# Kernel optimization log

Measured on AMD Instinct MI355X. Metric: run time of the kernel, lower is better.

## Reference

```python
import jax, jax.numpy as jnp
import numpy as np

B, L, D_MODEL = 16, 2048, 512
S, D_LLM = 1000, 1024
H, E = 8, 64  # n_heads, d_keys
D_OUT = 64


def setup_inputs() -> dict:
    key = jax.random.key(0)
    ks = jax.random.split(key, 11)
    sc = lambda d: 1.0 / np.sqrt(d)
    return {
        "target_embedding": jax.random.normal(ks[0], (B, L, D_MODEL), dtype=jnp.float32),
        "source_embedding": jax.random.normal(ks[1], (S, D_LLM), dtype=jnp.float32),
        "value_embedding": jax.random.normal(ks[2], (S, D_LLM), dtype=jnp.float32),
        "Wq": jax.random.normal(ks[3], (D_MODEL, H * E), dtype=jnp.float32) * sc(D_MODEL),
        "bq": jnp.zeros((H * E,), dtype=jnp.float32),
        "Wk": jax.random.normal(ks[4], (D_LLM, H * E), dtype=jnp.float32) * sc(D_LLM),
        "bk": jnp.zeros((H * E,), dtype=jnp.float32),
        "Wv": jax.random.normal(ks[5], (D_LLM, H * E), dtype=jnp.float32) * sc(D_LLM),
        "bv": jnp.zeros((H * E,), dtype=jnp.float32),
        "Wo": jax.random.normal(ks[6], (H * E, D_OUT), dtype=jnp.float32) * sc(H * E),
        "bo": jnp.zeros((D_OUT,), dtype=jnp.float32),
    }


def reference(target_embedding, source_embedding, value_embedding,
              Wq, bq, Wk, bk, Wv, bv, Wo, bo):
    # projections
    q = (target_embedding @ Wq + bq).reshape(B, L, H, E)   # blhe
    k = (source_embedding @ Wk + bk).reshape(S, H, E)      # she
    v = (value_embedding @ Wv + bv).reshape(S, H, E)       # she
    scale = 1.0 / jnp.sqrt(jnp.asarray(E, dtype=q.dtype))
    scores = jnp.einsum("blhe,she->bhls", q, k)            # (B,H,L,S)
    A = jax.nn.softmax(scale * scores, axis=-1)            # dropout in eval mode = identity
    out = jnp.einsum("bhls,she->blhe", A, v).reshape(B, L, H * E)
    return out @ Wo + bo                                    # (B,L,64)
```

## Files before the change

### kernel.cpp

```cpp
#include <hip/hip_runtime.h>

typedef __attribute__((ext_vector_type(4))) float  f32x4;
typedef __attribute__((ext_vector_type(8))) __bf16 bf16x8;
typedef __attribute__((ext_vector_type(4))) __bf16 bf16x4;

static __device__ __forceinline__ f32x4 mfma16(bf16x8 a, bf16x8 b, f32x4 c) {
  return __builtin_amdgcn_mfma_f32_16x16x32_bf16(a, b, c, 0, 0, 0);
}

typedef __attribute__((address_space(1))) const unsigned int* gas1_t;
typedef __attribute__((address_space(3))) unsigned int* las3_t;
static __device__ __forceinline__ void glds16(const void* g, void* l) {
  __builtin_amdgcn_global_load_lds((gas1_t)g, (las3_t)l, 16, 0, 0);
}

#define QSCALE 0.18033688011112042f

__global__ __launch_bounds__(256) void prep_w(
    const float* __restrict__ Wq, const float* __restrict__ Wk,
    const float* __restrict__ Wv, const float* __restrict__ Wo,
    __bf16* __restrict__ wqT, __bf16* __restrict__ wkT,
    __bf16* __restrict__ wvT, __bf16* __restrict__ woT) {
  int i = blockIdx.x * 256 + threadIdx.x;
  if (i < 262144) {
    int k = i & 511, n = i >> 9;
    wqT[i] = (__bf16)Wq[k * 512 + n];
  } else if (i < 786432) {
    int j = i - 262144; int k = j & 1023, n = j >> 10;
    wkT[j] = (__bf16)Wk[k * 512 + n];
  } else if (i < 1310720) {
    int j = i - 786432; int k = j & 1023, n = j >> 10;
    wvT[j] = (__bf16)Wv[k * 512 + n];
  } else if (i < 1343488) {
    int j = i - 1310720; int k = j & 511, n = j >> 9;
    woT[j] = (__bf16)Wo[k * 64 + n];
  }
}

__global__ __launch_bounds__(256) void prep_cvt(
    const float* __restrict__ tgt, const float* __restrict__ src,
    const float* __restrict__ val,
    __bf16* __restrict__ tgtb, __bf16* __restrict__ srcb, __bf16* __restrict__ valb) {
  const int j = blockIdx.x * 256 + threadIdx.x;
  const int C0 = 32768 * 512 / 4;
  const int CV = 1024 * 1024 / 4;
  if (j < C0) {
    f32x4 v = *(const f32x4*)&tgt[(size_t)j * 4];
    bf16x4 o; o[0]=(__bf16)v[0]; o[1]=(__bf16)v[1]; o[2]=(__bf16)v[2]; o[3]=(__bf16)v[3];
    *(bf16x4*)&tgtb[(size_t)j * 4] = o;
  } else if (j < C0 + 2 * CV) {
    const int which = (j - C0) / CV;
    const int u = (j - C0) - which * CV;
    const float* in = which ? val : src;
    __bf16* outp = which ? valb : srcb;
    bf16x4 o;
    if (u * 4 < 1000 * 1024) {
      f32x4 v = *(const f32x4*)&in[(size_t)u * 4];
      o[0]=(__bf16)v[0]; o[1]=(__bf16)v[1]; o[2]=(__bf16)v[2]; o[3]=(__bf16)v[3];
    } else {
      o[0]=(__bf16)0.0f; o[1]=(__bf16)0.0f; o[2]=(__bf16)0.0f; o[3]=(__bf16)0.0f;
    }
    *(bf16x4*)&outp[(size_t)u * 4] = o;
  }
}

template <int MODE>
__global__ __launch_bounds__(256, 2) void gemm_bt(
    const __bf16* __restrict__ A, const __bf16* __restrict__ BT,
    const float* __restrict__ bias, float scale,
    __bf16* __restrict__ C, int M, int N, int K) {
  const int n0 = blockIdx.x * 128, m0 = blockIdx.y * 128;
  __shared__ __bf16 sA[128 * 32], sB[128 * 32];
  const int t = threadIdx.x;
  const int w = t >> 6, lane = t & 63;
  const int wr = w >> 1, wc = w & 1;
  const int lr = lane & 15, lg = lane >> 4;

  const int grow = w * 32 + (lane >> 2);
  const int lslot = (lane & 3) ^ ((lane >> 2) & 3) ^ (lane >> 4);
  char* const sAw = (char*)sA + w * 2048;
  char* const sBw = (char*)sB + w * 2048;

  const int rslot = (lg ^ (lr & 3) ^ ((lr >> 2) & 3)) << 4;
  const int aOff = wr * 4096 + lr * 64 + rslot;
  const int bOff = wc * 4096 + lr * 64 + rslot;

  f32x4 acc[4][4];
#pragma unroll
  for (int i = 0; i < 4; ++i)
#pragma unroll
    for (int j = 0; j < 4; ++j) acc[i][j] = f32x4{0.f, 0.f, 0.f, 0.f};

  const size_t gaBase0 = (size_t)(m0 + grow) * K + lslot * 8;
  const size_t gaBase1 = (size_t)(m0 + grow + 16) * K + lslot * 8;
  const size_t gbBase0 = (size_t)(n0 + grow) * K + lslot * 8;
  const size_t gbBase1 = (size_t)(n0 + grow + 16) * K + lslot * 8;

  for (int kc = 0; kc < K; kc += 32) {
    __syncthreads();
    glds16(&A[gaBase0 + kc], sAw);
    glds16(&A[gaBase1 + kc], sAw + 1024);
    glds16(&BT[gbBase0 + kc], sBw);
    glds16(&BT[gbBase1 + kc], sBw + 1024);
    __syncthreads();

    bf16x8 af[4], bfr[4];
#pragma unroll
    for (int i = 0; i < 4; ++i) {
      af[i]  = *(const bf16x8*)((const char*)sA + aOff + i * 1024);
      bfr[i] = *(const bf16x8*)((const char*)sB + bOff + i * 1024);
    }
    __builtin_amdgcn_s_setprio(1);
#pragma unroll
    for (int i = 0; i < 4; ++i)
#pragma unroll
      for (int j = 0; j < 4; ++j) acc[i][j] = mfma16(af[i], bfr[j], acc[i][j]);
    __builtin_amdgcn_s_setprio(0);
  }

#pragma unroll
  for (int i = 0; i < 4; ++i) {
    const int rowb = m0 + wr * 64 + i * 16 + lg * 4;
#pragma unroll
    for (int j = 0; j < 4; ++j) {
      const int col = n0 + wc * 64 + j * 16 + lr;
      const float bb = bias ? bias[col] : 0.0f;
      if (MODE == 0) {
#pragma unroll
        for (int r = 0; r < 4; ++r)
          C[(size_t)(rowb + r) * N + col] = (__bf16)((acc[i][j][r] + bb) * scale);
      } else {
        bf16x4 v;
#pragma unroll
        for (int r = 0; r < 4; ++r) v[r] = (__bf16)((acc[i][j][r] + bb) * scale);
        *(bf16x4*)&C[(size_t)col * M + rowb] = v;
      }
    }
  }
}

__global__ __launch_bounds__(256) void attn_kernel(
    const __bf16* __restrict__ qg, const __bf16* __restrict__ kg,
    const __bf16* __restrict__ vtg, __bf16* __restrict__ og) {
  const int bid = blockIdx.x;
  const int lt = bid & 15, h = (bid >> 4) & 7, b = bid >> 7;
  const int w = threadIdx.x >> 6, lane = threadIdx.x & 63;
  const int lr = lane & 15, g = lane >> 4, lr7 = lane & 7;
  const int l0 = lt * 128 + w * 32;

  __shared__ __bf16 sK[2][4096];
  __shared__ __bf16 sV[2][4096];
  __shared__ __bf16 sP[4][2048];
  char* const pbase = (char*)&sP[w][0];

  const int srowi = lane >> 3;
  const int sslot = (lane & 7) ^ srowi;
  const int krow = w * 16 + srowi;
  const size_t kgBase = (size_t)krow * 512 + h * 64 + sslot * 8;
  const size_t vgBase = (size_t)(h * 64 + krow) * 1024 + sslot * 8;

  bf16x8 qf[2][2];
#pragma unroll
  for (int qi = 0; qi < 2; ++qi)
#pragma unroll
    for (int hf = 0; hf < 2; ++hf)
      qf[qi][hf] = *(const bf16x8*)&qg[
          ((size_t)b * 2048 + l0 + qi * 16 + lr) * 512 + h * 64 + hf * 32 + g * 8];

  f32x4 o[2][4];
#pragma unroll
  for (int qi = 0; qi < 2; ++qi)
#pragma unroll
    for (int j = 0; j < 4; ++j) o[qi][j] = f32x4{0.f, 0.f, 0.f, 0.f};
  float ls[2] = {0.f, 0.f};

  const int eOff0 = lr * 128 + ((g ^ lr7) << 4);
  const int pswz = lr7 << 4;

  glds16(&kg[kgBase], (char*)&sK[0][0] + w * 2048);
  glds16(&kg[kgBase + (size_t)8 * 512], (char*)&sK[0][0] + w * 2048 + 1024);
  glds16(&vtg[vgBase], (char*)&sV[0][0] + w * 2048);
  glds16(&vtg[vgBase + (size_t)8 * 1024], (char*)&sV[0][0] + w * 2048 + 1024);
  __syncthreads();

  for (int sc = 0; sc < 16; ++sc) {
    const int p = sc & 1;
    if (sc < 15) {
      const int sn = (sc + 1) * 64;
      char* nk = (char*)&sK[p ^ 1][0] + w * 2048;
      char* nv = (char*)&sV[p ^ 1][0] + w * 2048;
      glds16(&kg[kgBase + (size_t)sn * 512], nk);
      glds16(&kg[kgBase + (size_t)(sn + 8) * 512], nk + 1024);
      glds16(&vtg[vgBase + sn], nv);
      glds16(&vtg[vgBase + sn + 8 * 1024], nv + 1024);
    }
    const char* kbuf = (const char*)&sK[p][0];
    const char* vbuf = (const char*)&sV[p][0];

    bf16x8 kf[4][2];
#pragma unroll
    for (int t = 0; t < 4; ++t) {
      kf[t][0] = *(const bf16x8*)(kbuf + t * 2048 + eOff0);
      kf[t][1] = *(const bf16x8*)(kbuf + t * 2048 + (eOff0 ^ 64));
    }
    f32x4 d[2][4];
    __builtin_amdgcn_s_setprio(1);
#pragma unroll
    for (int qi = 0; qi < 2; ++qi)
#pragma unroll
      for (int t = 0; t < 4; ++t) {
        f32x4 z = {0.f, 0.f, 0.f, 0.f};
        z = mfma16(kf[t][0], qf[qi][0], z);
        z = mfma16(kf[t][1], qf[qi][1], z);
        d[qi][t] = z;
      }
    __builtin_amdgcn_s_setprio(0);
    if (sc == 15) {
#pragma unroll
      for (int qi = 0; qi < 2; ++qi)
#pragma unroll
        for (int t = 0; t < 4; ++t)
#pragma unroll
          for (int r = 0; r < 4; ++r)
            if (960 + t * 16 + 4 * g + r >= 1000) d[qi][t][r] = -1.0e30f;
    }

#pragma unroll
    for (int qi = 0; qi < 2; ++qi) {
#pragma unroll
      for (int t = 0; t < 4; ++t) {
        const float p0 = exp2f(d[qi][t][0]);
        const float p1 = exp2f(d[qi][t][1]);
        const float p2 = exp2f(d[qi][t][2]);
        const float p3 = exp2f(d[qi][t][3]);
        ls[qi] += (p0 + p1) + (p2 + p3);
        bf16x4 pv; pv[0]=(__bf16)p0; pv[1]=(__bf16)p1; pv[2]=(__bf16)p2; pv[3]=(__bf16)p3;
        *(bf16x4*)(pbase + qi * 2048 + lr * 128 + ((t * 32 + g * 8) ^ pswz)) = pv;
      }
    }

#pragma unroll
    for (int kc = 0; kc < 2; ++kc) {
      bf16x8 vf[4];
#pragma unroll
      for (int j = 0; j < 4; ++j)
        vf[j] = *(const bf16x8*)(vbuf + j * 2048 + (eOff0 ^ (kc * 64)));
#pragma unroll
      for (int qi = 0; qi < 2; ++qi) {
        const bf16x8 pf = *(const bf16x8*)(
            pbase + qi * 2048 + lr * 128 + ((kc * 64 + g * 16) ^ pswz));
        __builtin_amdgcn_s_setprio(1);
#pragma unroll
        for (int j = 0; j < 4; ++j)
          o[qi][j] = mfma16(pf, vf[j], o[qi][j]);
        __builtin_amdgcn_s_setprio(0);
      }
    }
    __syncthreads();
  }

#pragma unroll
  for (int qi = 0; qi < 2; ++qi) {
    float l = ls[qi];
    l += __shfl_xor(l, 16);
    l += __shfl_xor(l, 32);
    const float rinv = 1.0f / l;
    const float r0 = __shfl(rinv, 4 * g + 0);
    const float r1 = __shfl(rinv, 4 * g + 1);
    const float r2 = __shfl(rinv, 4 * g + 2);
    const float r3 = __shfl(rinv, 4 * g + 3);
    const size_t ob = ((size_t)b * 2048 + l0 + qi * 16) * 512 + h * 64;
#pragma unroll
    for (int j = 0; j < 4; ++j) {
      og[ob + (size_t)(4 * g + 0) * 512 + j * 16 + lr] = (__bf16)(o[qi][j][0] * r0);
      og[ob + (size_t)(4 * g + 1) * 512 + j * 16 + lr] = (__bf16)(o[qi][j][1] * r1);
      og[ob + (size_t)(4 * g + 2) * 512 + j * 16 + lr] = (__bf16)(o[qi][j][2] * r2);
      og[ob + (size_t)(4 * g + 3) * 512 + j * 16 + lr] = (__bf16)(o[qi][j][3] * r3);
    }
  }
}

__global__ __launch_bounds__(256) void out_proj(
    const __bf16* __restrict__ ab, const __bf16* __restrict__ woT,
    const float* __restrict__ bo, float* __restrict__ out) {
  const int w = threadIdx.x >> 6, lane = threadIdx.x & 63;
  const int lr = lane & 15, g = lane >> 4;
  const int r0 = blockIdx.x * 64 + w * 16;
  f32x4 acc[4];
#pragma unroll
  for (int j = 0; j < 4; ++j) acc[j] = f32x4{0.f, 0.f, 0.f, 0.f};
  for (int kc = 0; kc < 512; kc += 32) {
    const bf16x8 af = *(const bf16x8*)&ab[(size_t)(r0 + lr) * 512 + kc + g * 8];
#pragma unroll
    for (int j = 0; j < 4; ++j) {
      const bf16x8 bf = *(const bf16x8*)&woT[(size_t)(j * 16 + lr) * 512 + kc + g * 8];
      acc[j] = mfma16(af, bf, acc[j]);
    }
  }
#pragma unroll
  for (int j = 0; j < 4; ++j) {
    const int col = j * 16 + lr;
    const float bb = bo[col];
#pragma unroll
    for (int r = 0; r < 4; ++r)
      out[(size_t)(r0 + 4 * g + r) * 64 + col] = acc[j][r] + bb;
  }
}

extern "C" void kernel_launch(void* const* d_in, const int* in_sizes, int n_in,
                              void* d_out, int out_size, void* d_ws, size_t ws_size,
                              hipStream_t stream) {
  const float* tgt = (const float*)d_in[0];
  const float* src = (const float*)d_in[1];
  const float* val = (const float*)d_in[2];
  const float* Wq  = (const float*)d_in[3];
  const float* bq  = (const float*)d_in[4];
  const float* Wk  = (const float*)d_in[5];
  const float* bk  = (const float*)d_in[6];
  const float* Wv  = (const float*)d_in[7];
  const float* bv  = (const float*)d_in[8];
  const float* Wo  = (const float*)d_in[9];
  const float* bo  = (const float*)d_in[10];
  float* out = (float*)d_out;
  char* ws = (char*)d_ws;

  __bf16* wqT  = (__bf16*)(ws + 0);
  __bf16* wkT  = (__bf16*)(ws + 524288);
  __bf16* wvT  = (__bf16*)(ws + 1572864);
  __bf16* woT  = (__bf16*)(ws + 2621440);
  __bf16* srcb = (__bf16*)(ws + 2686976);
  __bf16* valb = (__bf16*)(ws + 4784128);
  __bf16* kb   = (__bf16*)(ws + 6881280);
  __bf16* vtb  = (__bf16*)(ws + 7929856);
  __bf16* tgtb = (__bf16*)(ws + 8978432);
  __bf16* attnb= (__bf16*)(ws + 8978432);
  __bf16* qb   = (__bf16*)(ws + 42532864);

  prep_w<<<5248, 256, 0, stream>>>(Wq, Wk, Wv, Wo, wqT, wkT, wvT, woT);
  prep_cvt<<<18432, 256, 0, stream>>>(tgt, src, val, tgtb, srcb, valb);

  gemm_bt<0><<<dim3(4, 256), 256, 0, stream>>>(tgtb, wqT, bq, QSCALE, qb, 32768, 512, 512);
  gemm_bt<0><<<dim3(4, 8), 256, 0, stream>>>(srcb, wkT, bk, 1.0f, kb, 1024, 512, 1024);
  gemm_bt<1><<<dim3(4, 8), 256, 0, stream>>>(valb, wvT, bv, 1.0f, vtb, 1024, 512, 1024);

  attn_kernel<<<2048, 256, 0, stream>>>(qb, kb, vtb, attnb);

  out_proj<<<512, 256, 0, stream>>>(attnb, woT, bo, out);
}
```

Measured before the change: 334.6 us.

## Use MFMA row-sum and transposed PV in attention, tile weight transpose

The attention kernel now swaps the operands of the PV MFMA so the output is produced transposed. This allows vectorized bf16x4 stores per row and removes the shuffle-based normalization. The softmax denominator is now computed by an extra MFMA against a ones vector rather than scalar adds. The P staging buffer is halved by processing one query block at a time, and launch bounds now request 4 blocks per CU. The weight-transpose prep kernel uses a shared-memory 32x32 tile so both its reads and writes are coalesced. The trade-offs are extra MFMA work and a denominator summed over bf16-rounded P values.

```diff
diff --git a/kernel.cpp b/kernel.cpp
--- a/kernel.cpp
+++ b/kernel.cpp
@@ -16,25 +16,27 @@
 
 #define QSCALE 0.18033688011112042f
 
-__global__ __launch_bounds__(256) void prep_w(
+__global__ __launch_bounds__(256) void prep_wT(
     const float* __restrict__ Wq, const float* __restrict__ Wk,
     const float* __restrict__ Wv, const float* __restrict__ Wo,
     __bf16* __restrict__ wqT, __bf16* __restrict__ wkT,
     __bf16* __restrict__ wvT, __bf16* __restrict__ woT) {
-  int i = blockIdx.x * 256 + threadIdx.x;
-  if (i < 262144) {
-    int k = i & 511, n = i >> 9;
-    wqT[i] = (__bf16)Wq[k * 512 + n];
-  } else if (i < 786432) {
-    int j = i - 262144; int k = j & 1023, n = j >> 10;
-    wkT[j] = (__bf16)Wk[k * 512 + n];
-  } else if (i < 1310720) {
-    int j = i - 786432; int k = j & 1023, n = j >> 10;
-    wvT[j] = (__bf16)Wv[k * 512 + n];
-  } else if (i < 1343488) {
-    int j = i - 1310720; int k = j & 511, n = j >> 9;
-    woT[j] = (__bf16)Wo[k * 64 + n];
-  }
+  __shared__ float tile[32][33];
+  const int t = blockIdx.x;
+  const float* in; __bf16* out; int K, N, tk, tn;
+  if (t < 256)       { in = Wq; out = wqT; K = 512;  N = 512; tk = t & 15;          tn = t >> 4; }
+  else if (t < 768)  { in = Wk; out = wkT; K = 1024; N = 512; tk = (t-256) & 31;    tn = (t-256) >> 5; }
+  else if (t < 1280) { in = Wv; out = wvT; K = 1024; N = 512; tk = (t-768) & 31;    tn = (t-768) >> 5; }
+  else               { in = Wo; out = woT; K = 512;  N = 64;  tk = (t-1280) & 15;   tn = (t-1280) >> 4; }
+  const int k0 = tk * 32, n0 = tn * 32;
+  const int c = threadIdx.x & 31, r = threadIdx.x >> 5;
+#pragma unroll
+  for (int i = 0; i < 4; ++i)
+    tile[r + i * 8][c] = in[(size_t)(k0 + r + i * 8) * N + n0 + c];
+  __syncthreads();
+#pragma unroll
+  for (int i = 0; i < 4; ++i)
+    out[(size_t)(n0 + r + i * 8) * K + k0 + c] = (__bf16)tile[c][r + i * 8];
 }
 
 __global__ __launch_bounds__(256) void prep_cvt(
@@ -139,7 +141,7 @@
   }
 }
 
-__global__ __launch_bounds__(256) void attn_kernel(
+__global__ __launch_bounds__(256, 4) void attn_kernel(
     const __bf16* __restrict__ qg, const __bf16* __restrict__ kg,
     const __bf16* __restrict__ vtg, __bf16* __restrict__ og) {
   const int bid = blockIdx.x;
@@ -150,7 +152,7 @@
 
   __shared__ __bf16 sK[2][4096];
   __shared__ __bf16 sV[2][4096];
-  __shared__ __bf16 sP[4][2048];
+  __shared__ __bf16 sP[4][1024];
   char* const pbase = (char*)&sP[w][0];
 
   const int srowi = lane >> 3;
@@ -167,12 +169,17 @@
       qf[qi][hf] = *(const bf16x8*)&qg[
           ((size_t)b * 2048 + l0 + qi * 16 + lr) * 512 + h * 64 + hf * 32 + g * 8];
 
-  f32x4 o[2][4];
-#pragma unroll
-  for (int qi = 0; qi < 2; ++qi)
+  f32x4 o[2][4], lsacc[2];
+#pragma unroll
+  for (int qi = 0; qi < 2; ++qi) {
 #pragma unroll
     for (int j = 0; j < 4; ++j) o[qi][j] = f32x4{0.f, 0.f, 0.f, 0.f};
-  float ls[2] = {0.f, 0.f};
+    lsacc[qi] = f32x4{0.f, 0.f, 0.f, 0.f};
+  }
+
+  bf16x8 ones8;
+#pragma unroll
+  for (int i = 0; i < 8; ++i) ones8[i] = (__bf16)1.0f;
 
   const int eOff0 = lr * 128 + ((g ^ lr7) << 4);
   const int pswz = lr7 << 4;
@@ -225,34 +232,33 @@
             if (960 + t * 16 + 4 * g + r >= 1000) d[qi][t][r] = -1.0e30f;
     }
 
+    bf16x8 vf[2][4];
+#pragma unroll
+    for (int kc = 0; kc < 2; ++kc)
+#pragma unroll
+      for (int j = 0; j < 4; ++j)
+        vf[kc][j] = *(const bf16x8*)(vbuf + j * 2048 + (eOff0 ^ (kc * 64)));
+
 #pragma unroll
     for (int qi = 0; qi < 2; ++qi) {
 #pragma unroll
       for (int t = 0; t < 4; ++t) {
-        const float p0 = exp2f(d[qi][t][0]);
-        const float p1 = exp2f(d[qi][t][1]);
-        const float p2 = exp2f(d[qi][t][2]);
-        const float p3 = exp2f(d[qi][t][3]);
-        ls[qi] += (p0 + p1) + (p2 + p3);
-        bf16x4 pv; pv[0]=(__bf16)p0; pv[1]=(__bf16)p1; pv[2]=(__bf16)p2; pv[3]=(__bf16)p3;
-        *(bf16x4*)(pbase + qi * 2048 + lr * 128 + ((t * 32 + g * 8) ^ pswz)) = pv;
+        bf16x4 pv;
+        pv[0] = (__bf16)exp2f(d[qi][t][0]);
+        pv[1] = (__bf16)exp2f(d[qi][t][1]);
+        pv[2] = (__bf16)exp2f(d[qi][t][2]);
+        pv[3] = (__bf16)exp2f(d[qi][t][3]);
+        *(bf16x4*)(pbase + lr * 128 + ((t * 32 + g * 8) ^ pswz)) = pv;
       }
-    }
-
-#pragma unroll
-    for (int kc = 0; kc < 2; ++kc) {
-      bf16x8 vf[4];
-#pragma unroll
-      for (int j = 0; j < 4; ++j)
-        vf[j] = *(const bf16x8*)(vbuf + j * 2048 + (eOff0 ^ (kc * 64)));
-#pragma unroll
-      for (int qi = 0; qi < 2; ++qi) {
-        const bf16x8 pf = *(const bf16x8*)(
-            pbase + qi * 2048 + lr * 128 + ((kc * 64 + g * 16) ^ pswz));
+#pragma unroll
+      for (int kc = 0; kc < 2; ++kc) {
+        const bf16x8 pB = *(const bf16x8*)(
+            pbase + lr * 128 + ((kc * 64 + g * 16) ^ pswz));
         __builtin_amdgcn_s_setprio(1);
+        lsacc[qi] = mfma16(ones8, pB, lsacc[qi]);
 #pragma unroll
         for (int j = 0; j < 4; ++j)
-          o[qi][j] = mfma16(pf, vf[j], o[qi][j]);
+          o[qi][j] = mfma16(vf[kc][j], pB, o[qi][j]);
         __builtin_amdgcn_s_setprio(0);
       }
     }
@@ -261,21 +267,14 @@
 
 #pragma unroll
   for (int qi = 0; qi < 2; ++qi) {
-    float l = ls[qi];
-    l += __shfl_xor(l, 16);
-    l += __shfl_xor(l, 32);
-    const float rinv = 1.0f / l;
-    const float r0 = __shfl(rinv, 4 * g + 0);
-    const float r1 = __shfl(rinv, 4 * g + 1);
-    const float r2 = __shfl(rinv, 4 * g + 2);
-    const float r3 = __shfl(rinv, 4 * g + 3);
-    const size_t ob = ((size_t)b * 2048 + l0 + qi * 16) * 512 + h * 64;
+    const float rinv = 1.0f / lsacc[qi][0];
+    const size_t rowb = ((size_t)b * 2048 + l0 + qi * 16 + lr) * 512 + h * 64;
 #pragma unroll
     for (int j = 0; j < 4; ++j) {
-      og[ob + (size_t)(4 * g + 0) * 512 + j * 16 + lr] = (__bf16)(o[qi][j][0] * r0);
-      og[ob + (size_t)(4 * g + 1) * 512 + j * 16 + lr] = (__bf16)(o[qi][j][1] * r1);
-      og[ob + (size_t)(4 * g + 2) * 512 + j * 16 + lr] = (__bf16)(o[qi][j][2] * r2);
-      og[ob + (size_t)(4 * g + 3) * 512 + j * 16 + lr] = (__bf16)(o[qi][j][3] * r3);
+      bf16x4 v;
+#pragma unroll
+      for (int r = 0; r < 4; ++r) v[r] = (__bf16)(o[qi][j][r] * rinv);
+      *(bf16x4*)&og[rowb + j * 16 + 4 * g] = v;
     }
   }
 }
@@ -336,7 +335,7 @@
   __bf16* attnb= (__bf16*)(ws + 8978432);
   __bf16* qb   = (__bf16*)(ws + 42532864);
 
-  prep_w<<<5248, 256, 0, stream>>>(Wq, Wk, Wv, Wo, wqT, wkT, wvT, woT);
+  prep_wT<<<1312, 256, 0, stream>>>(Wq, Wk, Wv, Wo, wqT, wkT, wvT, woT);
   prep_cvt<<<18432, 256, 0, stream>>>(tgt, src, val, tgtb, srcb, valb);
 
   gemm_bt<0><<<dim3(4, 256), 256, 0, stream>>>(tgtb, wqT, bq, QSCALE, qb, 32768, 512, 512);
```

Result: slower. 361.0 us (+7.9%).
